# Kernel optimization log

Measured on AMD Instinct MI355X. Metric: run time of the kernel, lower is better.

Reference implementation:

```python
import jax, jax.numpy as jnp
import numpy as np

B, T, D = 1, 2048, 768          # batch, seq_len, d_model
K, V = 8, 1024                   # n_codebooks, vocab_size
D_IN, D_STATE, D_CONV, DT_RANK = 1536, 16, 4, 48  # expand*d_model, ssm state, conv width, dt rank
L, SEG, RET_SCALE = 4, 256, 1.0  # n_layers, segment_size, retrieval_scale


def setup_inputs() -> dict:
    key = jax.random.key(0)
    ks = jax.random.split(key, 12)
    g = lambda k, shape, sc: jax.random.normal(k, shape, jnp.float32) * sc
    tokens = jax.random.randint(ks[0], (B, T, K), 0, V, dtype=jnp.int32)
    return dict(
        tokens=tokens,
        embed_w=g(ks[1], (K, V, D), 0.02),
        W_u=g(ks[2], (L, D, D), 1.0 / np.sqrt(D)),
        in_proj=g(ks[3], (L, 2 * D_IN, D), 1.0 / np.sqrt(D)),
        conv_w=g(ks[4], (L, D_IN, D_CONV), 0.5),
        conv_b=jnp.zeros((L, D_IN), jnp.float32),
        x_proj=g(ks[5], (L, DT_RANK + 2 * D_STATE, D_IN), 1.0 / np.sqrt(D_IN)),
        dt_w=g(ks[6], (L, D_IN, DT_RANK), 1.0 / np.sqrt(DT_RANK)),
        dt_b=jnp.full((L, D_IN), -4.0, jnp.float32),  # softplus(-4) ~ small init dt
        A_log=jnp.log(jnp.broadcast_to(jnp.arange(1.0, D_STATE + 1.0, dtype=jnp.float32), (L, D_IN, D_STATE))),
        D_skip=jnp.ones((L, D_IN), jnp.float32),
        out_proj=g(ks[7], (L, D, D_IN), 1.0 / np.sqrt(D_IN)),
        head_w=g(ks[8], (K, V, D), 0.02),
    )


def _mamba_block(x, in_proj, conv_w, conv_b, x_proj, dt_w, dt_b, A_log, D_skip, out_proj):
    # x: (B, T, D) -> (B, T, D). Canonical Mamba block with selective scan.
    xz = jnp.einsum('btd,ed->bte', x, in_proj)          # (B, T, 2*D_IN)
    u, z = xz[..., :D_IN], xz[..., D_IN:]
    # causal depthwise conv1d, kernel D_CONV
    up = jnp.pad(u, ((0, 0), (D_CONV - 1, 0), (0, 0)))
    u = sum(up[:, k:k + T, :] * conv_w[:, k] for k in range(D_CONV)) + conv_b
    u = jax.nn.silu(u)
    dbc = jnp.einsum('bte,fe->btf', u, x_proj)          # (B, T, DT_RANK + 2*D_STATE)
    dt_low = dbc[..., :DT_RANK]
    Bm = dbc[..., DT_RANK:DT_RANK + D_STATE]
    Cm = dbc[..., DT_RANK + D_STATE:]
    delta = jax.nn.softplus(jnp.einsum('btr,er->bte', dt_low, dt_w) + dt_b)  # (B, T, D_IN)
    A = -jnp.exp(A_log)                                  # (D_IN, D_STATE)

    def step(h, inp):
        d_t, B_t, C_t, u_t = inp                         # (B,D_IN),(B,D_STATE),(B,D_STATE),(B,D_IN)
        dA = jnp.exp(d_t[:, :, None] * A)
        h = dA * h + (d_t * u_t)[:, :, None] * B_t[:, None, :]
        y = jnp.einsum('bes,bs->be', h, C_t)
        return h, y

    h0 = jnp.zeros((B, D_IN, D_STATE), x.dtype)
    xs = (delta.transpose(1, 0, 2), Bm.transpose(1, 0, 2), Cm.transpose(1, 0, 2), u.transpose(1, 0, 2))
    _, ys = jax.lax.scan(jax.checkpoint(step), h0, xs)
    y = ys.transpose(1, 0, 2) + D_skip * u
    y = y * jax.nn.silu(z)
    return jnp.einsum('bte,de->btd', y, out_proj)


def _mc_block(x, W_u_l, mamba_params):
    # Memory-Cached Mamba block: mamba + within-sequence GRM segment retrieval.
    x_out = _mamba_block(x, *mamba_params)
    n_seg = T // SEG
    bpos = (jnp.arange(n_seg) + 1) * SEG - 1
    h_stack = x_out[:, bpos, :]                            # (B, N, D) boundary outputs (values)
    m_stack = x.reshape(B, n_seg, SEG, D).mean(axis=2)     # (B, N, D) segment means of inputs (keys)
    seg_idx = jnp.arange(T) // SEG
    mask = seg_idx[:, None] > jnp.arange(n_seg)[None, :]   # (T, N) causal over segments
    positions = jnp.arange(T)
    seg_starts = (positions // SEG) * SEG
    count = (positions - seg_starts + 1).astype(x.dtype)[None, :, None]
    cs = jnp.cumsum(x, axis=1)
    padded = jnp.concatenate([jnp.zeros((B, 1, D), x.dtype), cs], axis=1)
    m_current = (cs - padded[:, seg_starts, :]) / count    # running within-segment mean
    scale = 1.0 / np.sqrt(D)
    u = jnp.einsum('btd,ed->bte', x, W_u_l)
    sc = jnp.einsum('btd,bnd->btn', u, m_stack) * scale
    sc = jnp.where(mask[None], sc, -1e30)
    s_cur = jnp.sum(u * m_current, axis=-1, keepdims=True) * scale
    attn = jax.nn.softmax(jnp.concatenate([sc, s_cur], axis=-1), axis=-1)  # (B, T, N+1)
    h_ret = jnp.einsum('btn,bnd->btd', attn[..., :n_seg], h_stack)
    gate_cur = attn[..., n_seg:]
    return gate_cur * x_out + RET_SCALE * h_ret


def reference(tokens, embed_w, W_u, in_proj, conv_w, conv_b, x_proj, dt_w, dt_b, A_log, D_skip, out_proj, head_w):
    # RVQ embedding: sum of per-codebook embeddings
    x = embed_w[jnp.arange(K), tokens].sum(axis=2)         # (B, T, D)
    for l in range(L):
        mp = (in_proj[l], conv_w[l], conv_b[l], x_proj[l], dt_w[l], dt_b[l], A_log[l], D_skip[l], out_proj[l])
        x = _mc_block(x, W_u[l], mp)
    return jnp.einsum('btd,kvd->btkv', x, head_w)          # (B, T, K, V) per-codebook logits
```

## Files before the change

kernel.cpp:

```cpp
#include <hip/hip_runtime.h>
#include <hip/hip_bf16.h>


#define T_LEN   2048
#define DMODEL  768
#define DIN     1536
#define DXZ     3072
#define NSTATE  16
#define DTRANK  48
#define FDIM    80
#define NSEG    8
#define SEGLEN  256
#define NHEADV  8192
#define CH      64
#define NC      32

#define OFF_X     0u
#define OFF_XZ    1572864u
#define OFF_UC    7864320u
#define OFF_DBC   11010048u
#define OFF_DELTA 11173888u
#define OFF_Y     14319616u
#define OFF_XOUT  17465344u
#define OFF_URET  19038208u
#define OFF_MCUR  20611072u
#define OFF_MSTK  22183936u
#define OFF_WEMB  22190080u
#define OFF_WCW   28481536u
#define OFF_WCB   28506112u
#define OFF_WXP   28512256u
#define OFF_WDW   29003776u
#define OFF_WDB   29298688u
#define OFF_WAL   29304832u
#define OFF_WDS   29403136u
#define OFF_SLOC  29409280u
#define OFF_HIN   30195712u
#define OFF_CHP   30982144u
#define WS_TOTAL  31031296u
__device__ __align__(16) float g_ws[WS_TOTAL];

#define BF_XHI   0u
#define BF_XLO   1572864u
#define BF_YHI   3145728u
#define BF_YLO   6291456u
#define BF_IPHI  9437184u
#define BF_IPLO  18874368u
#define BF_OPHI  28311552u
#define BF_OPLO  33030144u
#define BF_WUHI  37748736u
#define BF_WULO  40108032u
#define BF_HWHI  42467328u
#define BF_HWLO  48758784u
#define BF_TOTAL 55050240u
__device__ __align__(16) unsigned short g_bf[BF_TOTAL];
__device__ unsigned int g_isbf16;

typedef __attribute__((ext_vector_type(8))) short bf16x8;
typedef __attribute__((ext_vector_type(4))) float f32x4;

__device__ __forceinline__ float bf2f(unsigned short u) {
  union { unsigned int i; float f; } c; c.i = ((unsigned int)u) << 16; return c.f;
}
__device__ __forceinline__ unsigned short f2bf(float f) {
  union { float f; unsigned int i; } c; c.f = f;
  unsigned int lsb = (c.i >> 16) & 1u;
  unsigned int r = c.i + 0x7fffu + lsb;
  return (unsigned short)(r >> 16);
}
__device__ __forceinline__ float softplusf(float v) {
  return v > 0.f ? v + log1pf(expf(-v)) : log1pf(expf(v));
}

__device__ __forceinline__ void gload16(const unsigned short* g, unsigned short* l) {
  __builtin_amdgcn_global_load_lds(
      (__attribute__((address_space(1))) unsigned int*)(unsigned long long)g,
      (__attribute__((address_space(3))) unsigned int*)(unsigned int)(unsigned long long)l,
      16, 0, 0);
}

__global__ void detect_kernel(const unsigned int* __restrict__ dsk) {
  if (threadIdx.x == 0 && blockIdx.x == 0)
    g_isbf16 = (dsk[0] == 0x3F803F80u) ? 1u : 0u;
}

__global__ __launch_bounds__(256) void convert_all(
    const void* __restrict__ s0, const void* __restrict__ s1,
    const void* __restrict__ s2, const void* __restrict__ s3,
    const void* __restrict__ s4, const void* __restrict__ s5,
    const void* __restrict__ s6, const void* __restrict__ s7) {
  int i = blockIdx.x * 256 + threadIdx.x;
  if (i >= 7219200) return;
  bool isb = (g_isbf16 != 0u);
  const void* src; unsigned dst; int j;
  if      (i < 6291456) { src = s0; dst = OFF_WEMB; j = i; }
  else if (i < 6316032) { src = s1; dst = OFF_WCW;  j = i - 6291456; }
  else if (i < 6322176) { src = s2; dst = OFF_WCB;  j = i - 6316032; }
  else if (i < 6813696) { src = s3; dst = OFF_WXP;  j = i - 6322176; }
  else if (i < 7108608) { src = s4; dst = OFF_WDW;  j = i - 6813696; }
  else if (i < 7114752) { src = s5; dst = OFF_WDB;  j = i - 7108608; }
  else if (i < 7213056) { src = s6; dst = OFF_WAL;  j = i - 7114752; }
  else                  { src = s7; dst = OFF_WDS;  j = i - 7213056; }
  float v = isb ? bf2f(((const unsigned short*)src)[j]) : ((const float*)src)[j];
  g_ws[dst + j] = v;
}

__global__ __launch_bounds__(256) void splitw_all(
    const void* __restrict__ s0, const void* __restrict__ s1,
    const void* __restrict__ s2, const void* __restrict__ s3) {
  int i = blockIdx.x * 256 + threadIdx.x;
  if (i >= 22806528) return;
  bool isb = (g_isbf16 != 0u);
  const void* src; unsigned hi, lo; int j;
  if      (i <  9437184) { src = s0; hi = BF_IPHI; lo = BF_IPLO; j = i; }
  else if (i < 14155776) { src = s1; hi = BF_OPHI; lo = BF_OPLO; j = i - 9437184; }
  else if (i < 16515072) { src = s2; hi = BF_WUHI; lo = BF_WULO; j = i - 14155776; }
  else                   { src = s3; hi = BF_HWHI; lo = BF_HWLO; j = i - 16515072; }
  float v = isb ? bf2f(((const unsigned short*)src)[j]) : ((const float*)src)[j];
  unsigned short h = f2bf(v);
  g_bf[hi + j] = h;
  g_bf[lo + j] = f2bf(v - bf2f(h));
}

__global__ __launch_bounds__(256) void split_act(
    unsigned srcoff, unsigned hioff, unsigned looff, int n) {
  int i = blockIdx.x * 256 + threadIdx.x;
  if (i >= n) return;
  float v = g_ws[srcoff + i];
  unsigned short h = f2bf(v);
  g_bf[hioff + i] = h;
  g_bf[looff + i] = f2bf(v - bf2f(h));
}

__global__ __launch_bounds__(256) void embed_kernel(const int* __restrict__ tokens) {
  int t = blockIdx.x;
  int tid = threadIdx.x;
  const float* __restrict__ emb = g_ws + OFF_WEMB;
  int tok[8];
#pragma unroll
  for (int k = 0; k < 8; ++k) tok[k] = tokens[t * 8 + k];
#pragma unroll
  for (int j = 0; j < 3; ++j) {
    int d = tid + j * 256;
    float s = 0.f;
#pragma unroll
    for (int k = 0; k < 8; ++k)
      s += emb[((size_t)k * 1024 + tok[k]) * DMODEL + d];
    g_ws[OFF_X + (size_t)t * DMODEL + d] = s;
  }
}

template <int BN, int EPI>
__global__ __launch_bounds__(256) void gemm_mfma(
    unsigned ahio, unsigned aloo, unsigned whio, unsigned wloo,
    unsigned coff, void* __restrict__ Cout, int ldc, int K) {
  constexpr int NWH = BN / 16;
  constexpr int NCH = 16 + 2 * NWH;
  constexpr int MI  = (BN == 128) ? 4 : 2;
  __shared__ __align__(16) unsigned short sA[2][2][128 * 32];
  __shared__ __align__(16) unsigned short sW[2][2][BN * 32];
  const unsigned short* __restrict__ ahi = g_bf + ahio;
  const unsigned short* __restrict__ alo = g_bf + aloo;
  const unsigned short* __restrict__ whi = g_bf + whio;
  const unsigned short* __restrict__ wlo = g_bf + wloo;
  int tid = threadIdx.x;
  int w = tid >> 6, lane = tid & 63;
  int lm = lane & 15, quad = lane >> 4;
  int bm = blockIdx.y * 128, bn = blockIdx.x * BN;
  int wr = (BN == 128) ? ((w >> 1) * 64) : (w * 32);
  int wc = (BN == 128) ? ((w & 1) * 64) : 0;
  int srow = lane & 15;
  int scol = (lane >> 4) * 8;
  f32x4 acc[MI][4] = {};

  auto stage = [&](int k0, int b) {
#pragma unroll
    for (int ci = 0; ci < NCH / 4; ++ci) {
      int ch = w + ci * 4;
      const unsigned short* src;
      unsigned short* dst;
      if (ch < 8) {
        src = ahi + (size_t)(bm + ch * 16 + srow) * K + k0 + scol;
        dst = &sA[b][0][ch * 512];
      } else if (ch < 16) {
        src = alo + (size_t)(bm + (ch - 8) * 16 + srow) * K + k0 + scol;
        dst = &sA[b][1][(ch - 8) * 512];
      } else if (ch < 16 + NWH) {
        src = whi + (size_t)(bn + (ch - 16) * 16 + srow) * K + k0 + scol;
        dst = &sW[b][0][(ch - 16) * 512];
      } else {
        src = wlo + (size_t)(bn + (ch - 16 - NWH) * 16 + srow) * K + k0 + scol;
        dst = &sW[b][1][(ch - 16 - NWH) * 512];
      }
      gload16(src, dst);
    }
  };

  int nk = K >> 5;
  stage(0, 0);
  __syncthreads();
  int cur = 0;
  int cA = wr >> 4, cW = wc >> 4;
  for (int t = 0; t < nk; ++t) {
    if (t + 1 < nk) stage((t + 1) << 5, cur ^ 1);
    bf16x8 ah[MI], al[MI], wh[4], wl[4];
#pragma unroll
    for (int mi = 0; mi < MI; ++mi) {
      ah[mi] = *(const bf16x8*)&sA[cur][0][(cA + mi) * 512 + lane * 8];
      al[mi] = *(const bf16x8*)&sA[cur][1][(cA + mi) * 512 + lane * 8];
    }
#pragma unroll
    for (int ni = 0; ni < 4; ++ni) {
      wh[ni] = *(const bf16x8*)&sW[cur][0][(cW + ni) * 512 + lane * 8];
      wl[ni] = *(const bf16x8*)&sW[cur][1][(cW + ni) * 512 + lane * 8];
    }
#pragma unroll
    for (int mi = 0; mi < MI; ++mi)
#pragma unroll
      for (int ni = 0; ni < 4; ++ni) {
        acc[mi][ni] = __builtin_amdgcn_mfma_f32_16x16x32_bf16(ah[mi], wh[ni], acc[mi][ni], 0, 0, 0);
        acc[mi][ni] = __builtin_amdgcn_mfma_f32_16x16x32_bf16(ah[mi], wl[ni], acc[mi][ni], 0, 0, 0);
        acc[mi][ni] = __builtin_amdgcn_mfma_f32_16x16x32_bf16(al[mi], wh[ni], acc[mi][ni], 0, 0, 0);
      }
    __syncthreads();
    cur ^= 1;
  }

  bool outb = (EPI == 2) && (g_isbf16 != 0u);
#pragma unroll
  for (int mi = 0; mi < MI; ++mi)
#pragma unroll
    for (int ni = 0; ni < 4; ++ni)
#pragma unroll
      for (int r = 0; r < 4; ++r) {
        int gm = bm + wr + mi * 16 + quad * 4 + r;
        int gn = bn + wc + ni * 16 + lm;
        float v = acc[mi][ni][r];
        if (EPI == 2) {
          if (outb) ((unsigned short*)Cout)[(size_t)gm * ldc + gn] = f2bf(v);
          else      ((float*)Cout)[(size_t)gm * ldc + gn] = v;
        } else {
          g_ws[coff + (size_t)gm * ldc + gn] = v;
        }
      }
}

template <int EPI>
__global__ __launch_bounds__(256) void gemm_nt(
    unsigned int aoff, int lda, unsigned int boff, int ldb,
    unsigned int coff, int ldc, int M, int N, int K, unsigned int biasoff) {
  const float* __restrict__ A = g_ws + aoff;
  const float* __restrict__ Bw = g_ws + boff;
  __shared__ float As[16][68];
  __shared__ float Bs[16][68];
  int tid = threadIdx.x;
  int bx = blockIdx.x, by = blockIdx.y;
  int tx = tid & 15, ty = tid >> 4;
  int lr = tid >> 2;
  int lc = (tid & 3) * 4;
  float acc[4][4] = {};
  for (int k0 = 0; k0 < K; k0 += 16) {
    const float* ap = A + (size_t)(by * 64 + lr) * lda + k0 + lc;
    float4 av = *reinterpret_cast<const float4*>(ap);
    As[lc + 0][lr] = av.x; As[lc + 1][lr] = av.y;
    As[lc + 2][lr] = av.z; As[lc + 3][lr] = av.w;
    int bn = bx * 64 + lr;
    float4 bv = make_float4(0.f, 0.f, 0.f, 0.f);
    if (bn < N)
      bv = *reinterpret_cast<const float4*>(Bw + (size_t)bn * ldb + k0 + lc);
    Bs[lc + 0][lr] = bv.x; Bs[lc + 1][lr] = bv.y;
    Bs[lc + 2][lr] = bv.z; Bs[lc + 3][lr] = bv.w;
    __syncthreads();
#pragma unroll
    for (int kk = 0; kk < 16; ++kk) {
      float4 a = *reinterpret_cast<const float4*>(&As[kk][ty * 4]);
      float4 b = *reinterpret_cast<const float4*>(&Bs[kk][tx * 4]);
      float ar[4] = {a.x, a.y, a.z, a.w};
      float br[4] = {b.x, b.y, b.z, b.w};
#pragma unroll
      for (int i = 0; i < 4; ++i)
#pragma unroll
        for (int j = 0; j < 4; ++j) acc[i][j] = fmaf(ar[i], br[j], acc[i][j]);
    }
    __syncthreads();
  }
  int m0 = by * 64 + ty * 4, n0 = bx * 64 + tx * 4;
#pragma unroll
  for (int i = 0; i < 4; ++i) {
#pragma unroll
    for (int j = 0; j < 4; ++j) {
      int m = m0 + i, n = n0 + j;
      if (n < N) {
        float v = acc[i][j];
        if (EPI == 1) v = softplusf(v + g_ws[biasoff + n]);
        g_ws[coff + (size_t)m * ldc + n] = v;
      }
    }
  }
}

__global__ __launch_bounds__(256) void conv_silu_kernel(
    unsigned int cwoff, unsigned int cboff) {
  int idx = blockIdx.x * 256 + threadIdx.x;
  int t = idx / DIN, e = idx - t * DIN;
  const float* __restrict__ xz = g_ws + OFF_XZ;
  const float* __restrict__ cw = g_ws + cwoff;
  float w0 = cw[e * 4 + 0], w1 = cw[e * 4 + 1];
  float w2 = cw[e * 4 + 2], w3 = cw[e * 4 + 3];
  float acc = g_ws[cboff + e];
  if (t >= 3) acc = fmaf(w0, xz[(size_t)(t - 3) * DXZ + e], acc);
  if (t >= 2) acc = fmaf(w1, xz[(size_t)(t - 2) * DXZ + e], acc);
  if (t >= 1) acc = fmaf(w2, xz[(size_t)(t - 1) * DXZ + e], acc);
  acc = fmaf(w3, xz[(size_t)t * DXZ + e], acc);
  float sig = 1.f / (1.f + __expf(-acc));
  g_ws[OFF_UC + idx] = acc * sig;
}

__global__ __launch_bounds__(256) void scan_phase1(unsigned int aloff) {
  int tid = threadIdx.x;
  int s = tid & 15;
  int e = blockIdx.x * 16 + (tid >> 4);
  int c = blockIdx.y;
  int t0 = c * CH;
  const float* __restrict__ delta = g_ws + OFF_DELTA;
  const float* __restrict__ uc    = g_ws + OFF_UC;
  const float* __restrict__ dbc   = g_ws + OFF_DBC;
  float a = -expf(g_ws[aloff + e * NSTATE + s]);
  float h = 0.f, P = 0.f;
  for (int i = 0; i < CH; ++i) {
    int t = t0 + i;
    float d = delta[(size_t)t * DIN + e];
    float u = uc[(size_t)t * DIN + e];
    float b = dbc[t * FDIM + DTRANK + s];
    float cc = dbc[t * FDIM + DTRANK + NSTATE + s];
    float dA = __expf(d * a);
    h = fmaf(dA, h, d * u * b);
    P += d;
    float yp = h * cc;
    yp += __shfl_xor(yp, 1);
    yp += __shfl_xor(yp, 2);
    yp += __shfl_xor(yp, 4);
    yp += __shfl_xor(yp, 8);
    if (s == 0) g_ws[OFF_Y + (size_t)t * DIN + e] = yp;
  }
  g_ws[OFF_SLOC + ((size_t)c * DIN + e) * NSTATE + s] = h;
  if (s == 0) g_ws[OFF_CHP + c * DIN + e] = P;
}

__global__ __launch_bounds__(256) void scan_phase2(unsigned int aloff) {
  int g = blockIdx.x * 256 + threadIdx.x;
  int e = g >> 4, s = g & 15;
  float a = -expf(g_ws[aloff + e * NSTATE + s]);
  float h = 0.f;
  for (int c = 0; c < NC; ++c) {
    g_ws[OFF_HIN + ((size_t)c * DIN + e) * NSTATE + s] = h;
    float S = g_ws[OFF_SLOC + ((size_t)c * DIN + e) * NSTATE + s];
    float P = g_ws[OFF_CHP + c * DIN + e];
    h = fmaf(__expf(a * P), h, S);
  }
}

__global__ __launch_bounds__(256) void scan_phase3(unsigned int aloff,
                                                   unsigned int dsoff) {
  int tid = threadIdx.x;
  int s = tid & 15;
  int e = blockIdx.x * 16 + (tid >> 4);
  int c = blockIdx.y;
  int t0 = c * CH;
  const float* __restrict__ delta = g_ws + OFF_DELTA;
  const float* __restrict__ uc    = g_ws + OFF_UC;
  const float* __restrict__ dbc   = g_ws + OFF_DBC;
  const float* __restrict__ xz    = g_ws + OFF_XZ;
  float a = -expf(g_ws[aloff + e * NSTATE + s]);
  float dsk = g_ws[dsoff + e];
  float hin = g_ws[OFF_HIN + ((size_t)c * DIN + e) * NSTATE + s];
  float P = 0.f;
  for (int i = 0; i < CH; ++i) {
    int t = t0 + i;
    float d = delta[(size_t)t * DIN + e];
    P += d;
    float cc = dbc[t * FDIM + DTRANK + NSTATE + s];
    float yp = __expf(a * P) * hin * cc;
    yp += __shfl_xor(yp, 1);
    yp += __shfl_xor(yp, 2);
    yp += __shfl_xor(yp, 4);
    yp += __shfl_xor(yp, 8);
    if (s == 0) {
      float u = uc[(size_t)t * DIN + e];
      float z = xz[(size_t)t * DXZ + DIN + e];
      float y = g_ws[OFF_Y + (size_t)t * DIN + e] + yp;
      float sig = 1.f / (1.f + __expf(-z));
      g_ws[OFF_Y + (size_t)t * DIN + e] = (y + dsk * u) * z * sig;
    }
  }
}

__global__ __launch_bounds__(256) void mcurrent_kernel() {
  int n = blockIdx.x / 3;
  int d = (blockIdx.x % 3) * 256 + threadIdx.x;
  const float* __restrict__ x = g_ws + OFF_X + (size_t)n * SEGLEN * DMODEL + d;
  float* __restrict__ mc = g_ws + OFF_MCUR + (size_t)n * SEGLEN * DMODEL + d;
  float run = 0.f;
  for (int i = 0; i < SEGLEN; ++i) {
    run += x[(size_t)i * DMODEL];
    mc[(size_t)i * DMODEL] = run / (float)(i + 1);
  }
}

__global__ __launch_bounds__(256) void retention_kernel() {
  int t = blockIdx.x;
  int tid = threadIdx.x;
  const float* __restrict__ xout = g_ws + OFF_XOUT;
  const float* __restrict__ uret = g_ws + OFF_URET;
  const float* __restrict__ mcur = g_ws + OFF_MCUR;
  __shared__ float red[4][9];
  __shared__ float attn_s[9];
  float p[9];
#pragma unroll
  for (int n = 0; n < 9; ++n) p[n] = 0.f;
#pragma unroll
  for (int j = 0; j < 3; ++j) {
    int d = tid + j * 256;
    float u = uret[(size_t)t * DMODEL + d];
    p[8] = fmaf(u, mcur[(size_t)t * DMODEL + d], p[8]);
#pragma unroll
    for (int n = 0; n < 8; ++n)
      p[n] = fmaf(u, mcur[(size_t)(n * SEGLEN + SEGLEN - 1) * DMODEL + d], p[n]);
  }
#pragma unroll
  for (int off = 32; off > 0; off >>= 1)
#pragma unroll
    for (int n = 0; n < 9; ++n) p[n] += __shfl_down(p[n], off, 64);
  int wave = tid >> 6;
  if ((tid & 63) == 0)
#pragma unroll
    for (int n = 0; n < 9; ++n) red[wave][n] = p[n];
  __syncthreads();
  if (tid == 0) {
    const float scale = 0.03608439182435161f;
    int seg = t >> 8;
    float sc[9], mx = -3.0e38f;
#pragma unroll
    for (int n = 0; n < 9; ++n) {
      float v = (red[0][n] + red[1][n] + red[2][n] + red[3][n]) * scale;
      if (n < 8 && n >= seg) v = -1e30f;
      sc[n] = v;
      mx = fmaxf(mx, v);
    }
    float den = 0.f;
#pragma unroll
    for (int n = 0; n < 9; ++n) {
      float e = __expf(sc[n] - mx);
      sc[n] = e;
      den += e;
    }
    float inv = 1.f / den;
#pragma unroll
    for (int n = 0; n < 9; ++n) attn_s[n] = sc[n] * inv;
  }
  __syncthreads();
  float a[9];
#pragma unroll
  for (int n = 0; n < 9; ++n) a[n] = attn_s[n];
#pragma unroll
  for (int j = 0; j < 3; ++j) {
    int d = tid + j * 256;
    float acc = a[8] * xout[(size_t)t * DMODEL + d];
#pragma unroll
    for (int n = 0; n < 8; ++n)
      acc = fmaf(a[n], xout[(size_t)(n * SEGLEN + SEGLEN - 1) * DMODEL + d], acc);
    g_ws[OFF_X + (size_t)t * DMODEL + d] = acc;
  }
}

extern "C" void kernel_launch(void* const* d_in, const int* in_sizes, int n_in,
                              void* d_out, int out_size, void* d_ws, size_t ws_size,
                              hipStream_t stream) {
  (void)in_sizes; (void)n_in; (void)out_size; (void)d_ws; (void)ws_size;
  const int* tokens = (const int*)d_in[0];

  detect_kernel<<<1, 64, 0, stream>>>((const unsigned int*)d_in[10]);

  convert_all<<<(7219200 + 255) / 256, 256, 0, stream>>>(
      d_in[1], d_in[4], d_in[5], d_in[6], d_in[7], d_in[8], d_in[9], d_in[10]);
  splitw_all<<<(22806528 + 255) / 256, 256, 0, stream>>>(
      d_in[3], d_in[11], d_in[2], d_in[12]);

  embed_kernel<<<T_LEN, 256, 0, stream>>>(tokens);

  for (int l = 0; l < 4; ++l) {
    unsigned int xp = OFF_WXP + (unsigned)l * FDIM * DIN;
    unsigned int dw = OFF_WDW + (unsigned)l * DIN * DTRANK;
    unsigned int db = OFF_WDB + (unsigned)l * DIN;
    unsigned int al = OFF_WAL + (unsigned)l * DIN * NSTATE;
    unsigned int ds = OFF_WDS + (unsigned)l * DIN;
    unsigned int cw = OFF_WCW + (unsigned)l * DIN * 4;
    unsigned int cb = OFF_WCB + (unsigned)l * DIN;
    unsigned int iphi = BF_IPHI + (unsigned)l * DXZ * DMODEL;
    unsigned int iplo = BF_IPLO + (unsigned)l * DXZ * DMODEL;
    unsigned int ophi = BF_OPHI + (unsigned)l * DMODEL * DIN;
    unsigned int oplo = BF_OPLO + (unsigned)l * DMODEL * DIN;
    unsigned int wuhi = BF_WUHI + (unsigned)l * DMODEL * DMODEL;
    unsigned int wulo = BF_WULO + (unsigned)l * DMODEL * DMODEL;

    split_act<<<(T_LEN * DMODEL) / 256, 256, 0, stream>>>(OFF_X, BF_XHI, BF_XLO,
                                                          T_LEN * DMODEL);
    gemm_mfma<128, 0><<<dim3(DXZ / 128, T_LEN / 128), 256, 0, stream>>>(
        BF_XHI, BF_XLO, iphi, iplo, OFF_XZ, nullptr, DXZ, DMODEL);
    conv_silu_kernel<<<(T_LEN * DIN) / 256, 256, 0, stream>>>(cw, cb);
    gemm_nt<0><<<dim3(2, 32), 256, 0, stream>>>(OFF_UC, DIN, xp, DIN,
                                                OFF_DBC, FDIM, T_LEN, FDIM, DIN, 0u);
    gemm_nt<1><<<dim3(24, 32), 256, 0, stream>>>(OFF_DBC, FDIM, dw, DTRANK,
                                                 OFF_DELTA, DIN, T_LEN, DIN, DTRANK, db);
    scan_phase1<<<dim3(DIN / 16, NC), 256, 0, stream>>>(al);
    scan_phase2<<<(DIN * NSTATE) / 256, 256, 0, stream>>>(al);
    scan_phase3<<<dim3(DIN / 16, NC), 256, 0, stream>>>(al, ds);
    split_act<<<(T_LEN * DIN) / 256, 256, 0, stream>>>(OFF_Y, BF_YHI, BF_YLO,
                                                       T_LEN * DIN);
    gemm_mfma<64, 0><<<dim3(DMODEL / 64, T_LEN / 128), 256, 0, stream>>>(
        BF_YHI, BF_YLO, ophi, oplo, OFF_XOUT, nullptr, DMODEL, DIN);
    mcurrent_kernel<<<NSEG * 3, 256, 0, stream>>>();
    gemm_mfma<64, 0><<<dim3(DMODEL / 64, T_LEN / 128), 256, 0, stream>>>(
        BF_XHI, BF_XLO, wuhi, wulo, OFF_URET, nullptr, DMODEL, DMODEL);
    retention_kernel<<<T_LEN, 256, 0, stream>>>();
  }

  split_act<<<(T_LEN * DMODEL) / 256, 256, 0, stream>>>(OFF_X, BF_XHI, BF_XLO,
                                                        T_LEN * DMODEL);
  gemm_mfma<128, 2><<<dim3(NHEADV / 128, T_LEN / 128), 256, 0, stream>>>(
      BF_XHI, BF_XLO, BF_HWHI, BF_HWLO, 0u, d_out, NHEADV, DMODEL);
}
```

Measured before the change: 2.498 ms.

## Fuse activation splits into producers, merge mid GEMMs, swizzle blocks, single-buffer LDS

The bf16 hi/lo split of activations now happens inside the embedding, scan phase3 and retention epilogues, which removes the separate split_act launches. The out_proj and W_u GEMMs are merged into one launch using grid z. GEMM blocks get an XCD-aware remap so neighbouring tiles land on the same die. The GEMM LDS double buffer is replaced by a single buffer with a sync before compute, which halves shared memory but gives up overlap of loads with MFMA work.

```diff
diff --git a/kernel.cpp b/kernel.cpp
--- a/kernel.cpp
+++ b/kernel.cpp
@@ -78,6 +78,14 @@
       16, 0, 0);
 }
 
+__device__ __forceinline__ void xcd_swz(int gx, int gy, int& bx, int& by) {
+  int flat = by * gx + bx;
+  int cpx = (gx * gy) >> 3;
+  int f2 = (flat & 7) * cpx + (flat >> 3);
+  bx = f2 % gx;
+  by = f2 / gx;
+}
+
 __global__ void detect_kernel(const unsigned int* __restrict__ dsk) {
   if (threadIdx.x == 0 && blockIdx.x == 0)
     g_isbf16 = (dsk[0] == 0x3F803F80u) ? 1u : 0u;
@@ -121,16 +129,6 @@
   g_bf[lo + j] = f2bf(v - bf2f(h));
 }
 
-__global__ __launch_bounds__(256) void split_act(
-    unsigned srcoff, unsigned hioff, unsigned looff, int n) {
-  int i = blockIdx.x * 256 + threadIdx.x;
-  if (i >= n) return;
-  float v = g_ws[srcoff + i];
-  unsigned short h = f2bf(v);
-  g_bf[hioff + i] = h;
-  g_bf[looff + i] = f2bf(v - bf2f(h));
-}
-
 __global__ __launch_bounds__(256) void embed_kernel(const int* __restrict__ tokens) {
   int t = blockIdx.x;
   int tid = threadIdx.x;
@@ -145,34 +143,35 @@
 #pragma unroll
     for (int k = 0; k < 8; ++k)
       s += emb[((size_t)k * 1024 + tok[k]) * DMODEL + d];
-    g_ws[OFF_X + (size_t)t * DMODEL + d] = s;
+    size_t idx = (size_t)t * DMODEL + d;
+    g_ws[OFF_X + idx] = s;
+    unsigned short h = f2bf(s);
+    g_bf[BF_XHI + idx] = h;
+    g_bf[BF_XLO + idx] = f2bf(s - bf2f(h));
   }
 }
 
 template <int BN, int EPI>
-__global__ __launch_bounds__(256) void gemm_mfma(
-    unsigned ahio, unsigned aloo, unsigned whio, unsigned wloo,
-    unsigned coff, void* __restrict__ Cout, int ldc, int K) {
+__device__ __forceinline__ void gemm_body(
+    const unsigned short* __restrict__ ahi, const unsigned short* __restrict__ alo,
+    const unsigned short* __restrict__ whi, const unsigned short* __restrict__ wlo,
+    unsigned coff, void* __restrict__ Cout, int ldc, int K, int bx, int by) {
   constexpr int NWH = BN / 16;
   constexpr int NCH = 16 + 2 * NWH;
   constexpr int MI  = (BN == 128) ? 4 : 2;
-  __shared__ __align__(16) unsigned short sA[2][2][128 * 32];
-  __shared__ __align__(16) unsigned short sW[2][2][BN * 32];
-  const unsigned short* __restrict__ ahi = g_bf + ahio;
-  const unsigned short* __restrict__ alo = g_bf + aloo;
-  const unsigned short* __restrict__ whi = g_bf + whio;
-  const unsigned short* __restrict__ wlo = g_bf + wloo;
+  __shared__ __align__(16) unsigned short sA[2][128 * 32];
+  __shared__ __align__(16) unsigned short sW[2][BN * 32];
   int tid = threadIdx.x;
   int w = tid >> 6, lane = tid & 63;
   int lm = lane & 15, quad = lane >> 4;
-  int bm = blockIdx.y * 128, bn = blockIdx.x * BN;
+  int bm = by * 128, bn = bx * BN;
   int wr = (BN == 128) ? ((w >> 1) * 64) : (w * 32);
   int wc = (BN == 128) ? ((w & 1) * 64) : 0;
   int srow = lane & 15;
   int scol = (lane >> 4) * 8;
+  int cA = wr >> 4, cW = wc >> 4;
   f32x4 acc[MI][4] = {};
-
-  auto stage = [&](int k0, int b) {
+  for (int k0 = 0; k0 < K; k0 += 32) {
 #pragma unroll
     for (int ci = 0; ci < NCH / 4; ++ci) {
       int ch = w + ci * 4;
@@ -180,38 +179,30 @@
       unsigned short* dst;
       if (ch < 8) {
         src = ahi + (size_t)(bm + ch * 16 + srow) * K + k0 + scol;
-        dst = &sA[b][0][ch * 512];
+        dst = &sA[0][ch * 512];
       } else if (ch < 16) {
         src = alo + (size_t)(bm + (ch - 8) * 16 + srow) * K + k0 + scol;
-        dst = &sA[b][1][(ch - 8) * 512];
+        dst = &sA[1][(ch - 8) * 512];
       } else if (ch < 16 + NWH) {
         src = whi + (size_t)(bn + (ch - 16) * 16 + srow) * K + k0 + scol;
-        dst = &sW[b][0][(ch - 16) * 512];
+        dst = &sW[0][(ch - 16) * 512];
       } else {
         src = wlo + (size_t)(bn + (ch - 16 - NWH) * 16 + srow) * K + k0 + scol;
-        dst = &sW[b][1][(ch - 16 - NWH) * 512];
+        dst = &sW[1][(ch - 16 - NWH) * 512];
       }
       gload16(src, dst);
     }
-  };
-
-  int nk = K >> 5;
-  stage(0, 0);
-  __syncthreads();
-  int cur = 0;
-  int cA = wr >> 4, cW = wc >> 4;
-  for (int t = 0; t < nk; ++t) {
-    if (t + 1 < nk) stage((t + 1) << 5, cur ^ 1);
+    __syncthreads();
     bf16x8 ah[MI], al[MI], wh[4], wl[4];
 #pragma unroll
     for (int mi = 0; mi < MI; ++mi) {
-      ah[mi] = *(const bf16x8*)&sA[cur][0][(cA + mi) * 512 + lane * 8];
-      al[mi] = *(const bf16x8*)&sA[cur][1][(cA + mi) * 512 + lane * 8];
+      ah[mi] = *(const bf16x8*)&sA[0][(cA + mi) * 512 + lane * 8];
+      al[mi] = *(const bf16x8*)&sA[1][(cA + mi) * 512 + lane * 8];
     }
 #pragma unroll
     for (int ni = 0; ni < 4; ++ni) {
-      wh[ni] = *(const bf16x8*)&sW[cur][0][(cW + ni) * 512 + lane * 8];
-      wl[ni] = *(const bf16x8*)&sW[cur][1][(cW + ni) * 512 + lane * 8];
+      wh[ni] = *(const bf16x8*)&sW[0][(cW + ni) * 512 + lane * 8];
+      wl[ni] = *(const bf16x8*)&sW[1][(cW + ni) * 512 + lane * 8];
     }
 #pragma unroll
     for (int mi = 0; mi < MI; ++mi)
@@ -222,9 +213,7 @@
         acc[mi][ni] = __builtin_amdgcn_mfma_f32_16x16x32_bf16(al[mi], wh[ni], acc[mi][ni], 0, 0, 0);
       }
     __syncthreads();
-    cur ^= 1;
-  }
-
+  }
   bool outb = (EPI == 2) && (g_isbf16 != 0u);
 #pragma unroll
   for (int mi = 0; mi < MI; ++mi)
@@ -242,6 +231,29 @@
           g_ws[coff + (size_t)gm * ldc + gn] = v;
         }
       }
+}
+
+template <int BN, int EPI>
+__global__ __launch_bounds__(256) void gemm_mfma(
+    unsigned ahio, unsigned aloo, unsigned whio, unsigned wloo,
+    unsigned coff, void* __restrict__ Cout, int ldc, int K) {
+  int bx = blockIdx.x, by = blockIdx.y;
+  xcd_swz(gridDim.x, gridDim.y, bx, by);
+  gemm_body<BN, EPI>(g_bf + ahio, g_bf + aloo, g_bf + whio, g_bf + wloo,
+                     coff, Cout, ldc, K, bx, by);
+}
+
+__global__ __launch_bounds__(256) void gemm_mid(
+    unsigned ophi, unsigned oplo, unsigned wuhi, unsigned wulo) {
+  int bx = blockIdx.x, by = blockIdx.y;
+  xcd_swz(gridDim.x, gridDim.y, bx, by);
+  if (blockIdx.z == 0) {
+    gemm_body<64, 0>(g_bf + BF_YHI, g_bf + BF_YLO, g_bf + ophi, g_bf + oplo,
+                     OFF_XOUT, nullptr, DMODEL, DIN, bx, by);
+  } else {
+    gemm_body<64, 0>(g_bf + BF_XHI, g_bf + BF_XLO, g_bf + wuhi, g_bf + wulo,
+                     OFF_URET, nullptr, DMODEL, DMODEL, bx, by);
+  }
 }
 
 template <int EPI>
@@ -389,7 +401,11 @@
       float z = xz[(size_t)t * DXZ + DIN + e];
       float y = g_ws[OFF_Y + (size_t)t * DIN + e] + yp;
       float sig = 1.f / (1.f + __expf(-z));
-      g_ws[OFF_Y + (size_t)t * DIN + e] = (y + dsk * u) * z * sig;
+      float v = (y + dsk * u) * z * sig;
+      size_t idx = (size_t)t * DIN + e;
+      unsigned short h = f2bf(v);
+      g_bf[BF_YHI + idx] = h;
+      g_bf[BF_YLO + idx] = f2bf(v - bf2f(h));
     }
   }
 }
@@ -468,7 +484,11 @@
 #pragma unroll
     for (int n = 0; n < 8; ++n)
       acc = fmaf(a[n], xout[(size_t)(n * SEGLEN + SEGLEN - 1) * DMODEL + d], acc);
-    g_ws[OFF_X + (size_t)t * DMODEL + d] = acc;
+    size_t idx = (size_t)t * DMODEL + d;
+    g_ws[OFF_X + idx] = acc;
+    unsigned short h = f2bf(acc);
+    g_bf[BF_XHI + idx] = h;
+    g_bf[BF_XLO + idx] = f2bf(acc - bf2f(h));
   }
 }
 
@@ -502,8 +522,6 @@
     unsigned int wuhi = BF_WUHI + (unsigned)l * DMODEL * DMODEL;
     unsigned int wulo = BF_WULO + (unsigned)l * DMODEL * DMODEL;
 
-    split_act<<<(T_LEN * DMODEL) / 256, 256, 0, stream>>>(OFF_X, BF_XHI, BF_XLO,
-                                                          T_LEN * DMODEL);
     gemm_mfma<128, 0><<<dim3(DXZ / 128, T_LEN / 128), 256, 0, stream>>>(
         BF_XHI, BF_XLO, iphi, iplo, OFF_XZ, nullptr, DXZ, DMODEL);
     conv_silu_kernel<<<(T_LEN * DIN) / 256, 256, 0, stream>>>(cw, cb);
@@ -514,18 +532,12 @@
     scan_phase1<<<dim3(DIN / 16, NC), 256, 0, stream>>>(al);
     scan_phase2<<<(DIN * NSTATE) / 256, 256, 0, stream>>>(al);
     scan_phase3<<<dim3(DIN / 16, NC), 256, 0, stream>>>(al, ds);
-    split_act<<<(T_LEN * DIN) / 256, 256, 0, stream>>>(OFF_Y, BF_YHI, BF_YLO,
-                                                       T_LEN * DIN);
-    gemm_mfma<64, 0><<<dim3(DMODEL / 64, T_LEN / 128), 256, 0, stream>>>(
-        BF_YHI, BF_YLO, ophi, oplo, OFF_XOUT, nullptr, DMODEL, DIN);
     mcurrent_kernel<<<NSEG * 3, 256, 0, stream>>>();
-    gemm_mfma<64, 0><<<dim3(DMODEL / 64, T_LEN / 128), 256, 0, stream>>>(
-        BF_XHI, BF_XLO, wuhi, wulo, OFF_URET, nullptr, DMODEL, DMODEL);
+    gemm_mid<<<dim3(DMODEL / 64, T_LEN / 128, 2), 256, 0, stream>>>(
+        ophi, oplo, wuhi, wulo);
     retention_kernel<<<T_LEN, 256, 0, stream>>>();
   }
 
-  split_act<<<(T_LEN * DMODEL) / 256, 256, 0, stream>>>(OFF_X, BF_XHI, BF_XLO,
-                                                        T_LEN * DMODEL);
   gemm_mfma<128, 2><<<dim3(NHEADV / 128, T_LEN / 128), 256, 0, stream>>>(
       BF_XHI, BF_XLO, BF_HWHI, BF_HWLO, 0u, d_out, NHEADV, DMODEL);
 }
```

Result: faster. 2.362 ms (-5.5%).
